# Kernel optimization log

Hardware: AMD Instinct MI355X
Metric: run time of the kernel (lower is better)

## Reference

```python
import jax, jax.numpy as jnp
import numpy as np

BATCH = 65536
VEC = 512       # CLIP embedding dim
K = 1024        # num_cluster
GAMMA = 0.99
EPS = 1e-05


def setup_inputs() -> dict:
    key = jax.random.key(0)
    k1, k2, k3 = jax.random.split(key, 3)
    batch_vectors = jax.random.normal(k1, (BATCH, VEC), dtype=jnp.float32)
    weight = jax.random.normal(k2, (VEC, K), dtype=jnp.float32)        # codebook, stored (vec_size, num_cluster)
    cluster_size = jnp.ones((K,), dtype=jnp.float32)
    embed_avg = jax.random.normal(k3, (VEC, K), dtype=jnp.float32)
    return {
        "batch_vectors": batch_vectors,
        "weight": weight,
        "cluster_size": cluster_size,
        "embed_avg": embed_avg,
    }


def reference(batch_vectors, weight, cluster_size, embed_avg):
    """One minibatch_update step of clusteringEMA_torch.

    Returns the updated codebook `weight` of shape (vec_size, num_cluster).
    """
    gamma = GAMMA
    eps = EPS
    num_cluster = weight.shape[1]

    # nearest centroid: squared L2 distance has the same argmin as the L2 norm
    x2 = jnp.sum(batch_vectors * batch_vectors, axis=1, keepdims=True)   # (B,1)
    w2 = jnp.sum(weight * weight, axis=0)[None, :]                       # (1,K)
    dist2 = x2 + w2 - 2.0 * (batch_vectors @ weight)                     # (B,K)
    argmin = jnp.argmin(dist2, axis=-1)                                  # (B,)

    # per-cluster counts (one-hot sum), zeros replaced by 1
    counts = jnp.zeros((num_cluster,), dtype=batch_vectors.dtype).at[argmin].add(1.0)
    n_idx_choice = jnp.where(counts == 0, 1.0, counts)

    # EMA of cluster sizes
    new_cluster_size = gamma * cluster_size + (1.0 - gamma) * n_idx_choice

    # embed_sum = x^T @ onehot  == per-cluster sum of assigned vectors, (vec,K)
    embed_sum = jax.ops.segment_sum(batch_vectors, argmin, num_segments=num_cluster).T
    new_embed_avg = gamma * embed_avg + (1.0 - gamma) * embed_sum

    # Laplace-smoothed normalization
    n = jnp.sum(new_cluster_size)
    cs = (new_cluster_size + eps) / (n + num_cluster * eps) * n
    new_weight = new_embed_avg / cs[None, :]
    return new_weight
```

## Files before the change

kernel.cpp:

```cpp
#include <hip/hip_runtime.h>

typedef unsigned int uint;
typedef unsigned short ushort_t;
typedef unsigned long long u64;
typedef __attribute__((ext_vector_type(4))) float f32x4;
typedef __attribute__((ext_vector_type(8))) __bf16 bf16x8;
typedef __attribute__((ext_vector_type(8))) unsigned short us8;

#define BATCH 65536
#define VEC 512
#define K 1024
#define GAMMA 0.99f
#define EPS 1e-05f
#define SEG 64
#define MARGIN 0.75f

#define NKT (VEC / 64)
#define TG 2048

__device__ __forceinline__ ushort_t rtn(float f) {
    uint u = __float_as_uint(f);
    return (ushort_t)((u + 0x7FFFu + ((u >> 16) & 1u)) >> 16);
}

__device__ __forceinline__ void gl16(const void* g, void* l) {
    __builtin_amdgcn_global_load_lds(
        (const __attribute__((address_space(1))) unsigned int*)g,
        (__attribute__((address_space(3))) unsigned int*)l, 16, 0, 0);
}

__device__ __forceinline__ float dec_key(uint e) {
    uint b = (e & 0x80000000u) ? (e & 0x7FFFFFFFu) : ~e;
    return __uint_as_float(b);
}

#define BC8(p) __builtin_bit_cast(bf16x8, (p))

__global__ void k_pack(const float* __restrict__ w, const float* __restrict__ x,
                       us8* __restrict__ wpk, us8* __restrict__ xpk,
                       float* __restrict__ wT, float* __restrict__ w2p,
                       int* __restrict__ cc ) {
    __shared__ float lds[32][257];
    const int b = blockIdx.x;
    const int t = threadIdx.x;

    if (b < 32) {
        const int gx = b >> 3, kt = b & 7;
        float s = 0.f;
#pragma unroll
        for (int ih = 0; ih < 2; ++ih) {
            __syncthreads();
#pragma unroll
            for (int r = 0; r < 32; ++r)
                lds[r][t] = w[(size_t)(kt * 64 + ih * 32 + r) * K + gx * 256 + t];
            __syncthreads();

#pragma unroll
            for (int r = 0; r < 32; ++r) { float f = lds[r][t]; s += f * f; }

#pragma unroll
            for (int i = 0; i < 4; ++i) {
                const int c = i * 256 + t;
                const int ct = c >> 6, lane = c & 63;
                const int cl = ct * 16 + (lane & 15);
                const int r0 = (lane >> 4) * 8;
                us8 v;
#pragma unroll
                for (int j = 0; j < 8; ++j) v[j] = rtn(lds[r0 + j][cl]);
                wpk[(size_t)b * TG + ct * 128 + ih * 64 + lane] = v;
            }

#pragma unroll
            for (int rr = 0; rr < 8; ++rr) {
                f32x4 v = {lds[rr * 4 + 0][t], lds[rr * 4 + 1][t],
                           lds[rr * 4 + 2][t], lds[rr * 4 + 3][t]};
                *(f32x4*)&wT[(size_t)(gx * 256 + t) * VEC + kt * 64 + ih * 32 + rr * 4] = v;
            }
        }
        w2p[kt * K + gx * 256 + t] = s;
        if (b < 8) cc[b * 256 + t] = 0;
    } else {
        const int blk = b - 32;
        const int gy = blk >> 3, kt = blk & 7;
#pragma unroll
        for (int i = 0; i < 8; ++i) {
            const int g = i * 256 + t;
            const int slab = g >> 7, ksub = (g >> 6) & 1, lane = g & 63;
            const int row = gy * 256 + slab * 16 + (lane & 15);
            const int k = kt * 64 + ksub * 32 + ((lane >> 4) << 3);
            const f32x4 q0 = *(const f32x4*)&x[(size_t)row * VEC + k];
            const f32x4 q1 = *(const f32x4*)&x[(size_t)row * VEC + k + 4];
            us8 v;
#pragma unroll
            for (int j = 0; j < 4; ++j) { v[j] = rtn(q0[j]); v[4 + j] = rtn(q1[j]); }
            xpk[(size_t)blk * TG + g] = v;
        }
    }
}

__launch_bounds__(512, 2)
__global__ void k_gemm(const us8* __restrict__ xpk, const us8* __restrict__ wpk,
                       const float* __restrict__ w2p,
                       u64* __restrict__ keysA, u64* __restrict__ keysB) {
    __shared__ us8 lds[2][2 * TG];

    const int blk = blockIdx.x;
    const int ord = blk >> 3;
    const int gy = (blk & 7) * 32 + (ord >> 2);
    const int gx = ord & 3;
    const int t = threadIdx.x;
    const int lane = t & 63;
    const int wv = t >> 6;
    const int wm = wv >> 2;
    const int wn = wv & 3;

    const us8* asrc = xpk + (size_t)gy * (NKT * TG);
    const us8* bsrc = wpk + (size_t)gx * (NKT * TG);

    auto stage = [&](int slot, int kt) {
        const us8* sa = asrc + (size_t)kt * TG;
        const us8* sb = bsrc + (size_t)kt * TG;
#pragma unroll
        for (int i = 0; i < 4; ++i) gl16(sa + i * 512 + t, &lds[slot][i * 512 + t]);
#pragma unroll
        for (int i = 0; i < 4; ++i) gl16(sb + i * 512 + t, &lds[slot][TG + i * 512 + t]);
    };

    f32x4 acc[8][4];
#pragma unroll
    for (int i = 0; i < 8; ++i)
#pragma unroll
        for (int j = 0; j < 4; ++j) acc[i][j] = (f32x4){0.f, 0.f, 0.f, 0.f};

    stage(0, 0);
    stage(1, 1);

    for (int kt = 0; kt < NKT; ++kt) {
        const int buf = kt & 1;
        if (kt + 1 < NKT) {
            if (kt >= 1) stage(buf ^ 1, kt + 1);
            asm volatile("s_waitcnt vmcnt(8)" ::: "memory");
        } else {
            asm volatile("s_waitcnt vmcnt(0)" ::: "memory");
        }
        __builtin_amdgcn_s_barrier();

#pragma unroll
        for (int ph = 0; ph < 2; ++ph) {
            const int kb = ph * 64;
            bf16x8 ah[8], bh[4];
#pragma unroll
            for (int rt = 0; rt < 8; ++rt)
                ah[rt] = BC8(lds[buf][(wm * 8 + rt) * 128 + kb + lane]);
#pragma unroll
            for (int ct = 0; ct < 4; ++ct)
                bh[ct] = BC8(lds[buf][TG + (wn * 4 + ct) * 128 + kb + lane]);
            __builtin_amdgcn_s_barrier();
            asm volatile("s_waitcnt lgkmcnt(0)" ::: "memory");
            __builtin_amdgcn_sched_barrier(0);
            __builtin_amdgcn_s_setprio(1);
#pragma unroll
            for (int rt = 0; rt < 8; ++rt)
#pragma unroll
                for (int ct = 0; ct < 4; ++ct)
                    acc[rt][ct] = __builtin_amdgcn_mfma_f32_16x16x32_bf16(ah[rt], bh[ct], acc[rt][ct], 0, 0, 0);
            __builtin_amdgcn_s_setprio(0);
            __builtin_amdgcn_s_barrier();
        }
    }

    const int col_base = gx * 256 + wn * 64;
    float w2c[4];
#pragma unroll
    for (int ct = 0; ct < 4; ++ct) {
        const int col = col_base + ct * 16 + (lane & 15);
        float s = 0.f;
#pragma unroll
        for (int p = 0; p < 8; ++p) s += w2p[p * K + col];
        w2c[ct] = s;
    }
    const int slot = gx * 4 + wn;

#pragma unroll
    for (int rt = 0; rt < 8; ++rt) {
#pragma unroll
        for (int reg = 0; reg < 4; ++reg) {
            u64 k1 = ~0ull, k2 = ~0ull;
#pragma unroll
            for (int ct = 0; ct < 4; ++ct) {
                float dist = w2c[ct] - 2.0f * acc[rt][ct][reg];
                uint su = __float_as_uint(dist);
                su = (su & 0x80000000u) ? ~su : (su | 0x80000000u);
                const u64 key = ((u64)su << 32) | (uint)(col_base + ct * 16 + (lane & 15));
                if (key < k1) { k2 = k1; k1 = key; }
                else if (key < k2) { k2 = key; }
            }
#pragma unroll
            for (int m = 1; m < 16; m <<= 1) {
                u64 o1 = __shfl_xor((unsigned long long)k1, m);
                u64 o2 = __shfl_xor((unsigned long long)k2, m);
                u64 lo = k1 < o1 ? k1 : o1;
                u64 hi = k1 < o1 ? o1 : k1;
                u64 mn2 = k2 < o2 ? k2 : o2;
                k1 = lo;
                k2 = hi < mn2 ? hi : mn2;
            }
            if ((lane & 15) == 0) {
                const int row = gy * 256 + wm * 128 + rt * 16 + (lane >> 4) * 4 + reg;
                keysA[(size_t)slot * BATCH + row] = k1;
                keysB[(size_t)slot * BATCH + row] = k2;
            }
        }
    }
}

__global__ void k_verify(const u64* __restrict__ keysA, const u64* __restrict__ keysB,
                         const float* __restrict__ x, const float* __restrict__ wT,
                         const float* __restrict__ w2p,
                         int* __restrict__ am, int* __restrict__ counts,
                         float* __restrict__ esum) {
    __shared__ int lrow[256];
    __shared__ int lcc[256];
    __shared__ int lcnt;
    const int t = threadIdx.x;
    const int r = blockIdx.x * 256 + t;
    const int lane = t & 63;

    if (t == 0) lcnt = 0;
    __syncthreads();

    f32x4 z = {0.f, 0.f, 0.f, 0.f};
    ((f32x4*)esum)[r * 2] = z;
    ((f32x4*)esum)[r * 2 + 1] = z;

    u64 m1 = ~0ull, s = ~0ull;
    int i1 = 0;
#pragma unroll
    for (int i = 0; i < 16; ++i) {
        u64 a = keysA[(size_t)i * BATCH + r];
        if (a < m1) { s = m1; m1 = a; i1 = i; }
        else if (a < s) s = a;
    }
    u64 b = keysB[(size_t)i1 * BATCH + r];
    u64 m2 = s < b ? s : b;

    const float d1 = dec_key((uint)(m1 >> 32));
    const float d2 = dec_key((uint)(m2 >> 32));
    const int c1 = (int)(uint)m1 & 1023;
    const int c2 = (int)(uint)m2 & 1023;

    if (d2 - d1 > MARGIN) {
        am[r] = c1;
        atomicAdd(&counts[c1], 1);
    } else {
        int p = atomicAdd(&lcnt, 1);
        lrow[p] = r;
        lcc[p] = (c1 << 10) | c2;
    }
    __syncthreads();

    const int n = lcnt;
    for (int idx = t >> 6; idx < n; idx += 4) {
        const int r2 = lrow[idx];
        const int cc1 = lcc[idx] >> 10;
        const int cc2 = lcc[idx] & 1023;
        const f32x4 x0 = *(const f32x4*)&x[(size_t)r2 * VEC + lane * 8];
        const f32x4 x1 = *(const f32x4*)&x[(size_t)r2 * VEC + lane * 8 + 4];
        float d[2];
        const int cand[2] = {cc1, cc2};
#pragma unroll
        for (int j = 0; j < 2; ++j) {
            const int c = cand[j];
            const f32x4 w0 = *(const f32x4*)&wT[(size_t)c * VEC + lane * 8];
            const f32x4 w1 = *(const f32x4*)&wT[(size_t)c * VEC + lane * 8 + 4];
            float p = x0[0] * w0[0] + x0[1] * w0[1] + x0[2] * w0[2] + x0[3] * w0[3]
                    + x1[0] * w1[0] + x1[1] * w1[1] + x1[2] * w1[2] + x1[3] * w1[3];
#pragma unroll
            for (int m = 1; m < 64; m <<= 1) p += __shfl_xor(p, m);
            float w2 = 0.f;
#pragma unroll
            for (int q = 0; q < 8; ++q) w2 += w2p[q * K + c];
            d[j] = w2 - 2.0f * p;
        }
        const int win = (d[0] < d[1] || (d[0] == d[1] && cc1 < cc2)) ? cc1 : cc2;
        if (lane == 0) {
            am[r2] = win;
            atomicAdd(&counts[win], 1);
        }
    }
}

__launch_bounds__(1024)
__global__ void k_scatter(const int* __restrict__ counts, const int* __restrict__ am,
                          int* __restrict__ cursor, int* __restrict__ sorted,
                          int* __restrict__ sortedk) {
    __shared__ int soff[K];
    __shared__ int wsum[16];
    const int t = threadIdx.x;
    const int lane = t & 63, wid = t >> 6;

    const int c = counts[t];
    int s = c;
#pragma unroll
    for (int d = 1; d < 64; d <<= 1) {
        int o = __shfl_up(s, d);
        if (lane >= d) s += o;
    }
    if (lane == 63) wsum[wid] = s;
    __syncthreads();
    if (wid == 0 && lane < 16) {
        int v = wsum[lane];
#pragma unroll
        for (int d = 1; d < 16; d <<= 1) {
            int o = __shfl_up(v, d);
            if (lane >= d) v += o;
        }
        wsum[lane] = v;
    }
    __syncthreads();
    soff[t] = (wid ? wsum[wid - 1] : 0) + s - c;
    __syncthreads();

    const int r = blockIdx.x * 1024 + t;
    const int k = am[r];
    const int pos = atomicAdd(&cursor[k], 1);
    sorted[soff[k] + pos] = r;
    sortedk[soff[k] + pos] = k;
}

__launch_bounds__(512)
__global__ void k_segred(const float* __restrict__ x, const int* __restrict__ sorted,
                         const int* __restrict__ sortedk, float* __restrict__ esum) {
    __shared__ int srow[SEG];
    __shared__ int skid[SEG];
    const int b = blockIdx.x;
    const int t = threadIdx.x;
    if (t < SEG) {
        srow[t] = sorted[b * SEG + t];
        skid[t] = sortedk[b * SEG + t];
    }
    __syncthreads();

    float a = 0.f;
    int cur = skid[0];
#pragma unroll 8
    for (int i = 0; i < SEG; ++i) {
        const int k = skid[i];
        if (k != cur) {
            atomicAdd(&esum[(size_t)cur * VEC + t], a);
            a = 0.f;
            cur = k;
        }
        a += x[(size_t)srow[i] * VEC + t];
    }
    atomicAdd(&esum[(size_t)cur * VEC + t], a);
}

__launch_bounds__(256)
__global__ void k_finalize(const float* __restrict__ esum, const float* __restrict__ embed_avg,
                           const int* __restrict__ counts,
                           const float* __restrict__ cluster_size,
                           float* __restrict__ out) {
    __shared__ float tile[64][65];
    __shared__ float wred[4];
    const int t = threadIdx.x;
    const int k0 = blockIdx.x * 64;
    const int v0 = blockIdx.y * 64;
    const int c = t & 63;
    const int r0 = t >> 6;
    const int lane = t & 63, wid = t >> 6;

    float part = 0.f;
#pragma unroll
    for (int j = 0; j < 4; ++j) {
        const int idx = t * 4 + j;
        const int cv = counts[idx];
        part += GAMMA * cluster_size[idx] + (1.0f - GAMMA) * ((cv == 0) ? 1.0f : (float)cv);
    }
#pragma unroll
    for (int d = 32; d > 0; d >>= 1) part += __shfl_xor(part, d);
    if (lane == 0) wred[wid] = part;

#pragma unroll
    for (int j = 0; j < 16; ++j) {
        const int r = r0 + j * 4;
        tile[r][c] = esum[(size_t)(k0 + r) * VEC + v0 + c];
    }
    __syncthreads();

    const float n = (wred[0] + wred[1]) + (wred[2] + wred[3]);
    const int kc = k0 + c;
    const int cv = counts[kc];
    const float ncs = GAMMA * cluster_size[kc] + (1.0f - GAMMA) * ((cv == 0) ? 1.0f : (float)cv);
    const float csk = (ncs + EPS) / (n + (float)K * EPS) * n;

#pragma unroll
    for (int j = 0; j < 16; ++j) {
        const int r = r0 + j * 4;
        const size_t o = (size_t)(v0 + r) * K + k0 + c;
        out[o] = (GAMMA * embed_avg[o] + (1.0f - GAMMA) * tile[c][r]) / csk;
    }
}

extern "C" void kernel_launch(void* const* d_in, const int* in_sizes, int n_in,
                              void* d_out, int out_size, void* d_ws, size_t ws_size,
                              hipStream_t stream) {
    const float* x            = (const float*)d_in[0];
    const float* w            = (const float*)d_in[1];
    const float* cluster_size = (const float*)d_in[2];
    const float* embed_avg    = (const float*)d_in[3];
    float* out = (float*)d_out;

    u64*   keysA   = (u64*)d_ws;
    u64*   keysB   = keysA + (size_t)16 * BATCH;
    int*   am      = (int*)(keysB + (size_t)16 * BATCH);
    float* w2p     = (float*)(am + BATCH);
    int*   cc      = (int*)(w2p + 8 * K);
    int*   counts  = cc;
    int*   cursor  = cc + K;
    int*   sorted  = cc + 2 * K;
    int*   sortedk = sorted + BATCH;
    float* esum    = (float*)(sortedk + BATCH);
    us8*   wpk     = (us8*)(esum + (size_t)K * VEC);
    float* wT      = (float*)(wpk + (size_t)32 * TG);
    us8*   xpk     = (us8*)(wT + (size_t)K * VEC);

    k_pack<<<2080, 256, 0, stream>>>(w, x, wpk, xpk, wT, w2p, cc);
    k_gemm<<<1024, 512, 0, stream>>>(xpk, wpk, w2p, keysA, keysB);
    k_verify<<<BATCH / 256, 256, 0, stream>>>(keysA, keysB, x, wT, w2p, am, counts, esum);
    k_scatter<<<64, 1024, 0, stream>>>(counts, am, cursor, sorted, sortedk);
    k_segred<<<BATCH / SEG, 512, 0, stream>>>(x, sorted, sortedk, esum);
    k_finalize<<<dim3(K / 64, VEC / 64), 256, 0, stream>>>(esum, embed_avg, counts, cluster_size, out);
}
```

Before: 407.2 us.

## Fuse x bf16 conversion into GEMM A-tile loading, drop xpk pre-pass

Removes the separate pass that converts the 128MB fp32 batch to a packed bf16 buffer. The GEMM now loads fp32 x into registers, rounds it to bf16 and writes it to LDS itself, with a register-staged prefetch one k-tile ahead. This saves a full write and reread of the packed A matrix, at the cost of more VGPRs, an extra barrier per k-tile and fp32 global reads inside the GEMM. SEG for the segment reduction is also halved, which doubles the number of segred blocks.

```diff
diff --git a/kernel.cpp b/kernel.cpp
--- a/kernel.cpp
+++ b/kernel.cpp
@@ -12,7 +12,7 @@
 #define K 1024
 #define GAMMA 0.99f
 #define EPS 1e-05f
-#define SEG 64
+#define SEG 32
 #define MARGIN 0.75f
 
 #define NKT (VEC / 64)
@@ -36,70 +36,52 @@
 
 #define BC8(p) __builtin_bit_cast(bf16x8, (p))
 
-__global__ void k_pack(const float* __restrict__ w, const float* __restrict__ x,
-                       us8* __restrict__ wpk, us8* __restrict__ xpk,
+__global__ void k_pack(const float* __restrict__ w, us8* __restrict__ wpk,
                        float* __restrict__ wT, float* __restrict__ w2p,
                        int* __restrict__ cc ) {
     __shared__ float lds[32][257];
     const int b = blockIdx.x;
-    const int t = threadIdx.x;
-
-    if (b < 32) {
-        const int gx = b >> 3, kt = b & 7;
-        float s = 0.f;
-#pragma unroll
-        for (int ih = 0; ih < 2; ++ih) {
-            __syncthreads();
-#pragma unroll
-            for (int r = 0; r < 32; ++r)
-                lds[r][t] = w[(size_t)(kt * 64 + ih * 32 + r) * K + gx * 256 + t];
-            __syncthreads();
-
-#pragma unroll
-            for (int r = 0; r < 32; ++r) { float f = lds[r][t]; s += f * f; }
-
-#pragma unroll
-            for (int i = 0; i < 4; ++i) {
-                const int c = i * 256 + t;
-                const int ct = c >> 6, lane = c & 63;
-                const int cl = ct * 16 + (lane & 15);
-                const int r0 = (lane >> 4) * 8;
-                us8 v;
-#pragma unroll
-                for (int j = 0; j < 8; ++j) v[j] = rtn(lds[r0 + j][cl]);
-                wpk[(size_t)b * TG + ct * 128 + ih * 64 + lane] = v;
-            }
-
-#pragma unroll
-            for (int rr = 0; rr < 8; ++rr) {
-                f32x4 v = {lds[rr * 4 + 0][t], lds[rr * 4 + 1][t],
-                           lds[rr * 4 + 2][t], lds[rr * 4 + 3][t]};
-                *(f32x4*)&wT[(size_t)(gx * 256 + t) * VEC + kt * 64 + ih * 32 + rr * 4] = v;
-            }
-        }
-        w2p[kt * K + gx * 256 + t] = s;
-        if (b < 8) cc[b * 256 + t] = 0;
-    } else {
-        const int blk = b - 32;
-        const int gy = blk >> 3, kt = blk & 7;
-#pragma unroll
-        for (int i = 0; i < 8; ++i) {
-            const int g = i * 256 + t;
-            const int slab = g >> 7, ksub = (g >> 6) & 1, lane = g & 63;
-            const int row = gy * 256 + slab * 16 + (lane & 15);
-            const int k = kt * 64 + ksub * 32 + ((lane >> 4) << 3);
-            const f32x4 q0 = *(const f32x4*)&x[(size_t)row * VEC + k];
-            const f32x4 q1 = *(const f32x4*)&x[(size_t)row * VEC + k + 4];
+    const int gx = b >> 3, kt = b & 7;
+    const int t = threadIdx.x;
+
+    float s = 0.f;
+#pragma unroll
+    for (int ih = 0; ih < 2; ++ih) {
+        __syncthreads();
+#pragma unroll
+        for (int r = 0; r < 32; ++r)
+            lds[r][t] = w[(size_t)(kt * 64 + ih * 32 + r) * K + gx * 256 + t];
+        __syncthreads();
+
+#pragma unroll
+        for (int r = 0; r < 32; ++r) { float f = lds[r][t]; s += f * f; }
+
+#pragma unroll
+        for (int i = 0; i < 4; ++i) {
+            const int c = i * 256 + t;
+            const int ct = c >> 6, lane = c & 63;
+            const int cl = ct * 16 + (lane & 15);
+            const int r0 = (lane >> 4) * 8;
             us8 v;
 #pragma unroll
-            for (int j = 0; j < 4; ++j) { v[j] = rtn(q0[j]); v[4 + j] = rtn(q1[j]); }
-            xpk[(size_t)blk * TG + g] = v;
-        }
-    }
+            for (int j = 0; j < 8; ++j) v[j] = rtn(lds[r0 + j][cl]);
+            wpk[(size_t)b * TG + ct * 128 + ih * 64 + lane] = v;
+        }
+
+#pragma unroll
+        for (int rr = 0; rr < 8; ++rr) {
+            f32x4 v = {lds[rr * 4 + 0][t], lds[rr * 4 + 1][t],
+                       lds[rr * 4 + 2][t], lds[rr * 4 + 3][t]};
+            *(f32x4*)&wT[(size_t)(gx * 256 + t) * VEC + kt * 64 + ih * 32 + rr * 4] = v;
+        }
+    }
+    w2p[kt * K + gx * 256 + t] = s;
+
+    if (b < 8) cc[b * 256 + t] = 0;
 }
 
 __launch_bounds__(512, 2)
-__global__ void k_gemm(const us8* __restrict__ xpk, const us8* __restrict__ wpk,
+__global__ void k_gemm(const float* __restrict__ x, const us8* __restrict__ wpk,
                        const float* __restrict__ w2p,
                        u64* __restrict__ keysA, u64* __restrict__ keysB) {
     __shared__ us8 lds[2][2 * TG];
@@ -114,14 +96,31 @@
     const int wm = wv >> 2;
     const int wn = wv & 3;
 
-    const us8* asrc = xpk + (size_t)gy * (NKT * TG);
     const us8* bsrc = wpk + (size_t)gx * (NKT * TG);
 
-    auto stage = [&](int slot, int kt) {
-        const us8* sa = asrc + (size_t)kt * TG;
+    f32x4 av[4][2];
+    auto aload = [&](int kt) {
+#pragma unroll
+        for (int i = 0; i < 4; ++i) {
+            const int g = t + i * 512;
+            const int row = gy * 256 + (g >> 7) * 16 + (g & 15);
+            const int k = kt * 64 + ((g >> 6) & 1) * 32 + (((g >> 4) & 3) << 3);
+            const float* p = x + (size_t)row * VEC + k;
+            av[i][0] = *(const f32x4*)p;
+            av[i][1] = *(const f32x4*)(p + 4);
+        }
+    };
+    auto awrite = [&](int slot) {
+#pragma unroll
+        for (int i = 0; i < 4; ++i) {
+            us8 v;
+#pragma unroll
+            for (int j = 0; j < 4; ++j) { v[j] = rtn(av[i][0][j]); v[4 + j] = rtn(av[i][1][j]); }
+            lds[slot][t + i * 512] = v;
+        }
+    };
+    auto bstage = [&](int slot, int kt) {
         const us8* sb = bsrc + (size_t)kt * TG;
-#pragma unroll
-        for (int i = 0; i < 4; ++i) gl16(sa + i * 512 + t, &lds[slot][i * 512 + t]);
 #pragma unroll
         for (int i = 0; i < 4; ++i) gl16(sb + i * 512 + t, &lds[slot][TG + i * 512 + t]);
     };
@@ -132,14 +131,21 @@
 #pragma unroll
         for (int j = 0; j < 4; ++j) acc[i][j] = (f32x4){0.f, 0.f, 0.f, 0.f};
 
-    stage(0, 0);
-    stage(1, 1);
+    aload(0);
+    bstage(0, 0);
+    awrite(0);
+    aload(1);
+    bstage(1, 1);
+    asm volatile("s_waitcnt lgkmcnt(0)" ::: "memory");
 
     for (int kt = 0; kt < NKT; ++kt) {
         const int buf = kt & 1;
-        if (kt + 1 < NKT) {
-            if (kt >= 1) stage(buf ^ 1, kt + 1);
-            asm volatile("s_waitcnt vmcnt(8)" ::: "memory");
+        if (kt >= 1 && kt + 1 < NKT) {
+            aload(kt + 1);
+            bstage(buf ^ 1, kt + 1);
+            asm volatile("s_waitcnt vmcnt(12)" ::: "memory");
+        } else if (kt == 0) {
+            asm volatile("s_waitcnt vmcnt(12)" ::: "memory");
         } else {
             asm volatile("s_waitcnt vmcnt(0)" ::: "memory");
         }
@@ -167,6 +173,10 @@
             __builtin_amdgcn_s_setprio(0);
             __builtin_amdgcn_s_barrier();
         }
+
+        if (kt + 1 < NKT) awrite(buf ^ 1);
+        asm volatile("s_waitcnt lgkmcnt(0)" ::: "memory");
+        __builtin_amdgcn_s_barrier();
     }
 
     const int col_base = gx * 256 + wn * 64;
@@ -423,10 +433,9 @@
     float* esum    = (float*)(sortedk + BATCH);
     us8*   wpk     = (us8*)(esum + (size_t)K * VEC);
     float* wT      = (float*)(wpk + (size_t)32 * TG);
-    us8*   xpk     = (us8*)(wT + (size_t)K * VEC);
-
-    k_pack<<<2080, 256, 0, stream>>>(w, x, wpk, xpk, wT, w2p, cc);
-    k_gemm<<<1024, 512, 0, stream>>>(xpk, wpk, w2p, keysA, keysB);
+
+    k_pack<<<32, 256, 0, stream>>>(w, wpk, wT, w2p, cc);
+    k_gemm<<<1024, 512, 0, stream>>>(x, wpk, w2p, keysA, keysB);
     k_verify<<<BATCH / 256, 256, 0, stream>>>(keysA, keysB, x, wT, w2p, am, counts, esum);
     k_scatter<<<64, 1024, 0, stream>>>(counts, am, cursor, sorted, sortedk);
     k_segred<<<BATCH / SEG, 512, 0, stream>>>(x, sorted, sortedk, esum);
```

Measured after the change: 435.2 us. 6.9% more time.
